# Kernel tuning notes

Hardware: AMD Instinct MI355X
Metric: run time of the kernel (lower is better)

The kernel has to match this reference:

```python
import jax, jax.numpy as jnp
import numpy as np

T, B, I, H = 512, 64, 256, 512

def setup_inputs() -> dict:
    key = jax.random.key(0)
    ks = jax.random.split(key, 5)
    s = 0.1  # matches uniform(-0.1, 0.1) init scale
    return {
        "x": jax.random.normal(ks[0], (T, B, I), dtype=jnp.float32),
        "weight_ih": jax.random.uniform(ks[1], (H, I), dtype=jnp.float32, minval=-s, maxval=s),
        "weight_hh": jax.random.uniform(ks[2], (H, H), dtype=jnp.float32, minval=-s, maxval=s),
        "bias_ih": jax.random.uniform(ks[3], (H,), dtype=jnp.float32, minval=-s, maxval=s),
        "bias_hh": jax.random.uniform(ks[4], (H,), dtype=jnp.float32, minval=-s, maxval=s),
    }

def reference(x, weight_ih, weight_hh, bias_ih, bias_hh):
    # Precompute input contribution for all timesteps in one big GEMM: [T,B,H]
    xw = jnp.einsum('tbi,hi->tbh', x, weight_ih) + bias_ih + bias_hh
    h0 = jnp.zeros((x.shape[1], weight_hh.shape[0]), dtype=x.dtype)

    def step(h, xw_t):
        h = jax.nn.relu(xw_t + h @ weight_hh.T)
        return h, h

    h_final, output = jax.lax.scan(step, h0, xw)
    return output, h_final
```

## Files before the change

### kernel.cpp

```cpp
#include <hip/hip_runtime.h>

#define T_DIM 512
#define B_DIM 64
#define I_DIM 256
#define H_DIM 512
#define BH_DIM (B_DIM * H_DIM)

__global__ __launch_bounds__(512, 2) void rnn_fused(
    const float* __restrict__ x, const float* __restrict__ wih,
    const float* __restrict__ whh, const float* __restrict__ bih,
    const float* __restrict__ bhh, float* __restrict__ out,
    unsigned long long* __restrict__ stage) {
  __shared__ __align__(16) float4 wihs4[128 * 64];
  __shared__ __align__(16) float hbuf[2][H_DIM];
  __shared__ __align__(16) float4 xbuf4[3 * 64];

  const int b   = blockIdx.x & 63;
  const int rb  = blockIdx.x >> 6;
  const int tid = threadIdx.x;
  const int rg  = tid >> 4;
  const int cg  = tid & 15;
  const int j0  = rb * 128 + rg * 4;

  const int pj = (tid < rb * 128) ? tid : tid + 128;

  float4 w[4][8];
#pragma unroll
  for (int r = 0; r < 4; r++) {
    const float4* wr = (const float4*)(whh + (size_t)(j0 + r) * H_DIM);
#pragma unroll
    for (int i = 0; i < 8; i++) w[r][i] = wr[i * 16 + cg];
  }

  {
    const float4* wg = (const float4*)(wih + (size_t)rb * 128 * I_DIM);
#pragma unroll
    for (int q = 0; q < 16; q++) {
      const int idx = q * 512 + tid;
      wihs4[idx] = wg[idx];
    }
  }

  const float4* xg = (const float4*)x;
  if (tid < 64) {
    xbuf4[0 * 64 + tid] = xg[((size_t)0 * B_DIM + b) * 64 + tid];
    xbuf4[1 * 64 + tid] = xg[((size_t)1 * B_DIM + b) * 64 + tid];
  }

  float bias = 0.f;
  if (cg < 4) bias = bih[j0 + cg] + bhh[j0 + cg];

  float* __restrict__ outb = out + (size_t)b * H_DIM;
  unsigned long long* __restrict__ stg0 = stage + (size_t)b * H_DIM;
  unsigned long long* __restrict__ stg1 = stage + (size_t)(64 + b) * H_DIM;

  __syncthreads();

  float hlast = 0.f;

  {
    float b0 = 0.f, b1 = 0.f, b2 = 0.f, b3 = 0.f;
    const float4* xb = &xbuf4[0];
    const float4* wr = &wihs4[(rg * 4) * 64];
#pragma unroll
    for (int i = 0; i < 4; i++) {
      const float4 xv = xb[i * 16 + cg];
      const float4 q0 = wr[0 * 64 + i * 16 + cg];
      const float4 q1 = wr[1 * 64 + i * 16 + cg];
      const float4 q2 = wr[2 * 64 + i * 16 + cg];
      const float4 q3 = wr[3 * 64 + i * 16 + cg];
      b0 = fmaf(q0.x, xv.x, b0); b0 = fmaf(q0.y, xv.y, b0);
      b0 = fmaf(q0.z, xv.z, b0); b0 = fmaf(q0.w, xv.w, b0);
      b1 = fmaf(q1.x, xv.x, b1); b1 = fmaf(q1.y, xv.y, b1);
      b1 = fmaf(q1.z, xv.z, b1); b1 = fmaf(q1.w, xv.w, b1);
      b2 = fmaf(q2.x, xv.x, b2); b2 = fmaf(q2.y, xv.y, b2);
      b2 = fmaf(q2.z, xv.z, b2); b2 = fmaf(q2.w, xv.w, b2);
      b3 = fmaf(q3.x, xv.x, b3); b3 = fmaf(q3.y, xv.y, b3);
      b3 = fmaf(q3.z, xv.z, b3); b3 = fmaf(q3.w, xv.w, b3);
    }
#pragma unroll
    for (int m = 1; m <= 8; m <<= 1) {
      b0 += __shfl_xor(b0, m, 64);
      b1 += __shfl_xor(b1, m, 64);
      b2 += __shfl_xor(b2, m, 64);
      b3 += __shfl_xor(b3, m, 64);
    }
    if (cg < 4) {
      const float acc = (cg == 0) ? b0 : (cg == 1) ? b1 : (cg == 2) ? b2 : b3;
      const float h = fmaxf(acc + bias, 0.f);
      const int j = j0 + cg;
      union { float f; unsigned int u; } cv; cv.f = h;
      __hip_atomic_store(&stg0[j], (unsigned long long)cv.u,
                         __ATOMIC_RELAXED, __HIP_MEMORY_SCOPE_AGENT);
      outb[j] = h;
      hbuf[0][j] = h;
      hlast = h;
    }
    if (tid < 64) {
      xbuf4[2 * 64 + tid] = xg[((size_t)2 * B_DIM + b) * 64 + tid];
    }
  }

  for (int t = 1; t < T_DIM; t++) {
    const int p = (t - 1) & 1;
    float* hb = hbuf[p];
    float* o_t = outb + (size_t)t * BH_DIM;

    float b0 = 0.f, b1 = 0.f, b2 = 0.f, b3 = 0.f;
    {
      const float4* xb = &xbuf4[(t % 3) * 64];
      const float4* wr = &wihs4[(rg * 4) * 64];
#pragma unroll
      for (int i = 0; i < 4; i++) {
        const float4 xv = xb[i * 16 + cg];
        const float4 q0 = wr[0 * 64 + i * 16 + cg];
        const float4 q1 = wr[1 * 64 + i * 16 + cg];
        const float4 q2 = wr[2 * 64 + i * 16 + cg];
        const float4 q3 = wr[3 * 64 + i * 16 + cg];
        b0 = fmaf(q0.x, xv.x, b0); b0 = fmaf(q0.y, xv.y, b0);
        b0 = fmaf(q0.z, xv.z, b0); b0 = fmaf(q0.w, xv.w, b0);
        b1 = fmaf(q1.x, xv.x, b1); b1 = fmaf(q1.y, xv.y, b1);
        b1 = fmaf(q1.z, xv.z, b1); b1 = fmaf(q1.w, xv.w, b1);
        b2 = fmaf(q2.x, xv.x, b2); b2 = fmaf(q2.y, xv.y, b2);
        b2 = fmaf(q2.z, xv.z, b2); b2 = fmaf(q2.w, xv.w, b2);
        b3 = fmaf(q3.x, xv.x, b3); b3 = fmaf(q3.y, xv.y, b3);
        b3 = fmaf(q3.z, xv.z, b3); b3 = fmaf(q3.w, xv.w, b3);
      }
    }

    float4 xpf = make_float4(0.f, 0.f, 0.f, 0.f);
    const bool do_pf = (tid < 64) && (t + 2 < T_DIM);
    if (do_pf) xpf = xg[((size_t)(t + 2) * B_DIM + b) * 64 + tid];

    if (tid < 384) {
      unsigned long long* slot = (p ? stg1 : stg0) + pj;
      const unsigned int want = (unsigned int)(t - 1);
      unsigned long long v;
      do {
        v = __hip_atomic_load(slot, __ATOMIC_RELAXED, __HIP_MEMORY_SCOPE_AGENT);
      } while ((unsigned int)(v >> 32) != want);
      union { unsigned int u; float f; } cv; cv.u = (unsigned int)v;
      hb[pj] = cv.f;
    }

    __syncthreads();

    if (do_pf) xbuf4[((t + 2) % 3) * 64 + tid] = xpf;

    float a0 = b0, a1 = b1, a2 = b2, a3 = b3;
#pragma unroll
    for (int i = 0; i < 8; i++) {
      const float4 hv = ((const float4*)hb)[i * 16 + cg];
      a0 = fmaf(w[0][i].x, hv.x, a0); a0 = fmaf(w[0][i].y, hv.y, a0);
      a0 = fmaf(w[0][i].z, hv.z, a0); a0 = fmaf(w[0][i].w, hv.w, a0);
      a1 = fmaf(w[1][i].x, hv.x, a1); a1 = fmaf(w[1][i].y, hv.y, a1);
      a1 = fmaf(w[1][i].z, hv.z, a1); a1 = fmaf(w[1][i].w, hv.w, a1);
      a2 = fmaf(w[2][i].x, hv.x, a2); a2 = fmaf(w[2][i].y, hv.y, a2);
      a2 = fmaf(w[2][i].z, hv.z, a2); a2 = fmaf(w[2][i].w, hv.w, a2);
      a3 = fmaf(w[3][i].x, hv.x, a3); a3 = fmaf(w[3][i].y, hv.y, a3);
      a3 = fmaf(w[3][i].z, hv.z, a3); a3 = fmaf(w[3][i].w, hv.w, a3);
    }
#pragma unroll
    for (int m = 1; m <= 8; m <<= 1) {
      a0 += __shfl_xor(a0, m, 64);
      a1 += __shfl_xor(a1, m, 64);
      a2 += __shfl_xor(a2, m, 64);
      a3 += __shfl_xor(a3, m, 64);
    }

    if (cg < 4) {
      const float acc = (cg == 0) ? a0 : (cg == 1) ? a1 : (cg == 2) ? a2 : a3;
      const float h = fmaxf(acc + bias, 0.f);
      const int j = j0 + cg;
      union { float f; unsigned int u; } cv; cv.f = h;
      const unsigned long long tag = (unsigned long long)(unsigned int)t << 32;
      unsigned long long* sb = (t & 1) ? stg1 : stg0;
      __hip_atomic_store(&sb[j], tag | cv.u,
                         __ATOMIC_RELAXED, __HIP_MEMORY_SCOPE_AGENT);
      o_t[j] = h;
      hbuf[t & 1][j] = h;
      hlast = h;
    }
  }

  if (cg < 4) {
    out[(size_t)T_DIM * BH_DIM + (size_t)b * H_DIM + j0 + cg] = hlast;
  }
}

extern "C" void kernel_launch(void* const* d_in, const int* in_sizes, int n_in,
                              void* d_out, int out_size, void* d_ws, size_t ws_size,
                              hipStream_t stream) {
  const float* x   = (const float*)d_in[0];
  const float* wih = (const float*)d_in[1];
  const float* whh = (const float*)d_in[2];
  const float* bih = (const float*)d_in[3];
  const float* bhh = (const float*)d_in[4];
  float* out = (float*)d_out;
  unsigned long long* stage = (unsigned long long*)d_ws;

  rnn_fused<<<256, 512, 0, stream>>>(x, wih, whh, bih, bhh, out, stage);
}
```

Measured before the change: 939.1 us.

## Split hidden rows into 8 slices and interleave two batch rows per block

Each block now owns 64 hidden rows (8 row-blocks) for two batch elements instead of 128 rows for one. The two batch recurrences alternate within the step: the wait and matvec for batch A run, then those for batch B. This halves the per-block recurrent matvec work on the critical path and lets one batch's cross-block wait overlap the other's compute. The cost is more blocks to synchronise per batch row, more polling threads, two barriers per step and a wider shuffle reduction.

```diff
diff --git a/kernel.cpp b/kernel.cpp
--- a/kernel.cpp
+++ b/kernel.cpp
@@ -6,185 +6,266 @@
 #define H_DIM 512
 #define BH_DIM (B_DIM * H_DIM)
 
-__global__ __launch_bounds__(512, 2) void rnn_fused(
+__global__ __launch_bounds__(512, 2) void rnn_fused2(
     const float* __restrict__ x, const float* __restrict__ wih,
     const float* __restrict__ whh, const float* __restrict__ bih,
     const float* __restrict__ bhh, float* __restrict__ out,
     unsigned long long* __restrict__ stage) {
-  __shared__ __align__(16) float4 wihs4[128 * 64];
-  __shared__ __align__(16) float hbuf[2][H_DIM];
-  __shared__ __align__(16) float4 xbuf4[3 * 64];
-
-  const int b   = blockIdx.x & 63;
-  const int rb  = blockIdx.x >> 6;
+  __shared__ __align__(16) float4 wihs4[64 * 64];
+  __shared__ __align__(16) float hbuf[2][2][H_DIM];
+  __shared__ __align__(16) float4 xbuf4[2][3][64];
+
+  const int bg  = blockIdx.x & 31;
+  const int rb  = blockIdx.x >> 5;
+  const int bA  = bg;
+  const int bB  = bg + 32;
   const int tid = threadIdx.x;
-  const int rg  = tid >> 4;
-  const int cg  = tid & 15;
-  const int j0  = rb * 128 + rg * 4;
-
-  const int pj = (tid < rb * 128) ? tid : tid + 128;
-
-  float4 w[4][8];
+  const int rg  = tid >> 5;
+  const int cg  = tid & 31;
+  const int j0  = rb * 64 + rg * 4;
+
+  const int pj = (tid < rb * 64) ? tid : tid + 64;
+
+  float4 w[4][4];
 #pragma unroll
   for (int r = 0; r < 4; r++) {
     const float4* wr = (const float4*)(whh + (size_t)(j0 + r) * H_DIM);
 #pragma unroll
-    for (int i = 0; i < 8; i++) w[r][i] = wr[i * 16 + cg];
+    for (int i = 0; i < 4; i++) w[r][i] = wr[i * 32 + cg];
   }
 
   {
-    const float4* wg = (const float4*)(wih + (size_t)rb * 128 * I_DIM);
-#pragma unroll
-    for (int q = 0; q < 16; q++) {
-      const int idx = q * 512 + tid;
-      wihs4[idx] = wg[idx];
-    }
+    const float4* wg = (const float4*)(wih + (size_t)rb * 64 * I_DIM);
+#pragma unroll
+    for (int q = 0; q < 8; q++) wihs4[q * 512 + tid] = wg[q * 512 + tid];
   }
 
   const float4* xg = (const float4*)x;
-  if (tid < 64) {
-    xbuf4[0 * 64 + tid] = xg[((size_t)0 * B_DIM + b) * 64 + tid];
-    xbuf4[1 * 64 + tid] = xg[((size_t)1 * B_DIM + b) * 64 + tid];
+  if (tid < 128) {
+    const int ab = tid >> 6;
+    const int c  = tid & 63;
+    const int bb = ab ? bB : bA;
+    xbuf4[ab][0][c] = xg[((size_t)0 * B_DIM + bb) * 64 + c];
+    xbuf4[ab][1][c] = xg[((size_t)1 * B_DIM + bb) * 64 + c];
   }
 
   float bias = 0.f;
   if (cg < 4) bias = bih[j0 + cg] + bhh[j0 + cg];
 
-  float* __restrict__ outb = out + (size_t)b * H_DIM;
-  unsigned long long* __restrict__ stg0 = stage + (size_t)b * H_DIM;
-  unsigned long long* __restrict__ stg1 = stage + (size_t)(64 + b) * H_DIM;
+  float* __restrict__ outA = out + (size_t)bA * H_DIM;
+  float* __restrict__ outB = out + (size_t)bB * H_DIM;
+  unsigned long long* __restrict__ stgA0 = stage + (size_t)bA * H_DIM;
+  unsigned long long* __restrict__ stgA1 = stage + (size_t)(64 + bA) * H_DIM;
+  unsigned long long* __restrict__ stgB0 = stage + (size_t)bB * H_DIM;
+  unsigned long long* __restrict__ stgB1 = stage + (size_t)(64 + bB) * H_DIM;
 
   __syncthreads();
 
-  float hlast = 0.f;
+  float hlastA = 0.f, hlastB = 0.f;
 
   {
-    float b0 = 0.f, b1 = 0.f, b2 = 0.f, b3 = 0.f;
-    const float4* xb = &xbuf4[0];
+    float aA0 = 0.f, aA1 = 0.f, aA2 = 0.f, aA3 = 0.f;
+    float aB0 = 0.f, aB1 = 0.f, aB2 = 0.f, aB3 = 0.f;
     const float4* wr = &wihs4[(rg * 4) * 64];
-#pragma unroll
-    for (int i = 0; i < 4; i++) {
-      const float4 xv = xb[i * 16 + cg];
-      const float4 q0 = wr[0 * 64 + i * 16 + cg];
-      const float4 q1 = wr[1 * 64 + i * 16 + cg];
-      const float4 q2 = wr[2 * 64 + i * 16 + cg];
-      const float4 q3 = wr[3 * 64 + i * 16 + cg];
-      b0 = fmaf(q0.x, xv.x, b0); b0 = fmaf(q0.y, xv.y, b0);
-      b0 = fmaf(q0.z, xv.z, b0); b0 = fmaf(q0.w, xv.w, b0);
-      b1 = fmaf(q1.x, xv.x, b1); b1 = fmaf(q1.y, xv.y, b1);
-      b1 = fmaf(q1.z, xv.z, b1); b1 = fmaf(q1.w, xv.w, b1);
-      b2 = fmaf(q2.x, xv.x, b2); b2 = fmaf(q2.y, xv.y, b2);
-      b2 = fmaf(q2.z, xv.z, b2); b2 = fmaf(q2.w, xv.w, b2);
-      b3 = fmaf(q3.x, xv.x, b3); b3 = fmaf(q3.y, xv.y, b3);
-      b3 = fmaf(q3.z, xv.z, b3); b3 = fmaf(q3.w, xv.w, b3);
-    }
-#pragma unroll
-    for (int m = 1; m <= 8; m <<= 1) {
-      b0 += __shfl_xor(b0, m, 64);
-      b1 += __shfl_xor(b1, m, 64);
-      b2 += __shfl_xor(b2, m, 64);
-      b3 += __shfl_xor(b3, m, 64);
+    const float4* xa = &xbuf4[0][0][0];
+    const float4* xb = &xbuf4[1][0][0];
+#pragma unroll
+    for (int i = 0; i < 2; i++) {
+      const int q = i * 32 + cg;
+      const float4 xva = xa[q];
+      const float4 xvb = xb[q];
+      const float4 q0 = wr[0 * 64 + q];
+      const float4 q1 = wr[1 * 64 + q];
+      const float4 q2 = wr[2 * 64 + q];
+      const float4 q3 = wr[3 * 64 + q];
+      aA0 = fmaf(q0.x, xva.x, aA0); aA0 = fmaf(q0.y, xva.y, aA0);
+      aA0 = fmaf(q0.z, xva.z, aA0); aA0 = fmaf(q0.w, xva.w, aA0);
+      aA1 = fmaf(q1.x, xva.x, aA1); aA1 = fmaf(q1.y, xva.y, aA1);
+      aA1 = fmaf(q1.z, xva.z, aA1); aA1 = fmaf(q1.w, xva.w, aA1);
+      aA2 = fmaf(q2.x, xva.x, aA2); aA2 = fmaf(q2.y, xva.y, aA2);
+      aA2 = fmaf(q2.z, xva.z, aA2); aA2 = fmaf(q2.w, xva.w, aA2);
+      aA3 = fmaf(q3.x, xva.x, aA3); aA3 = fmaf(q3.y, xva.y, aA3);
+      aA3 = fmaf(q3.z, xva.z, aA3); aA3 = fmaf(q3.w, xva.w, aA3);
+      aB0 = fmaf(q0.x, xvb.x, aB0); aB0 = fmaf(q0.y, xvb.y, aB0);
+      aB0 = fmaf(q0.z, xvb.z, aB0); aB0 = fmaf(q0.w, xvb.w, aB0);
+      aB1 = fmaf(q1.x, xvb.x, aB1); aB1 = fmaf(q1.y, xvb.y, aB1);
+      aB1 = fmaf(q1.z, xvb.z, aB1); aB1 = fmaf(q1.w, xvb.w, aB1);
+      aB2 = fmaf(q2.x, xvb.x, aB2); aB2 = fmaf(q2.y, xvb.y, aB2);
+      aB2 = fmaf(q2.z, xvb.z, aB2); aB2 = fmaf(q2.w, xvb.w, aB2);
+      aB3 = fmaf(q3.x, xvb.x, aB3); aB3 = fmaf(q3.y, xvb.y, aB3);
+      aB3 = fmaf(q3.z, xvb.z, aB3); aB3 = fmaf(q3.w, xvb.w, aB3);
+    }
+#pragma unroll
+    for (int m = 1; m <= 16; m <<= 1) {
+      aA0 += __shfl_xor(aA0, m, 64); aA1 += __shfl_xor(aA1, m, 64);
+      aA2 += __shfl_xor(aA2, m, 64); aA3 += __shfl_xor(aA3, m, 64);
+      aB0 += __shfl_xor(aB0, m, 64); aB1 += __shfl_xor(aB1, m, 64);
+      aB2 += __shfl_xor(aB2, m, 64); aB3 += __shfl_xor(aB3, m, 64);
     }
     if (cg < 4) {
-      const float acc = (cg == 0) ? b0 : (cg == 1) ? b1 : (cg == 2) ? b2 : b3;
-      const float h = fmaxf(acc + bias, 0.f);
       const int j = j0 + cg;
-      union { float f; unsigned int u; } cv; cv.f = h;
-      __hip_atomic_store(&stg0[j], (unsigned long long)cv.u,
-                         __ATOMIC_RELAXED, __HIP_MEMORY_SCOPE_AGENT);
-      outb[j] = h;
-      hbuf[0][j] = h;
-      hlast = h;
-    }
-    if (tid < 64) {
-      xbuf4[2 * 64 + tid] = xg[((size_t)2 * B_DIM + b) * 64 + tid];
+      union { float f; unsigned int u; } cv;
+      const float accA = (cg == 0) ? aA0 : (cg == 1) ? aA1 : (cg == 2) ? aA2 : aA3;
+      const float hA = fmaxf(accA + bias, 0.f);
+      cv.f = hA;
+      __hip_atomic_store(&stgA0[j], (unsigned long long)cv.u,
+                         __ATOMIC_RELAXED, __HIP_MEMORY_SCOPE_AGENT);
+      outA[j] = hA; hbuf[0][0][j] = hA; hlastA = hA;
+      const float accB = (cg == 0) ? aB0 : (cg == 1) ? aB1 : (cg == 2) ? aB2 : aB3;
+      const float hB = fmaxf(accB + bias, 0.f);
+      cv.f = hB;
+      __hip_atomic_store(&stgB0[j], (unsigned long long)cv.u,
+                         __ATOMIC_RELAXED, __HIP_MEMORY_SCOPE_AGENT);
+      outB[j] = hB; hbuf[1][0][j] = hB; hlastB = hB;
+    }
+    if (tid < 128) {
+      const int ab = tid >> 6;
+      const int c  = tid & 63;
+      const int bb = ab ? bB : bA;
+      xbuf4[ab][2][c] = xg[((size_t)2 * B_DIM + bb) * 64 + c];
     }
   }
 
   for (int t = 1; t < T_DIM; t++) {
     const int p = (t - 1) & 1;
-    float* hb = hbuf[p];
-    float* o_t = outb + (size_t)t * BH_DIM;
-
-    float b0 = 0.f, b1 = 0.f, b2 = 0.f, b3 = 0.f;
+    const int s = t % 3;
+    float* o_tA = outA + (size_t)t * BH_DIM;
+    float* o_tB = outB + (size_t)t * BH_DIM;
+
+    float aA0 = 0.f, aA1 = 0.f, aA2 = 0.f, aA3 = 0.f;
+    float aB0 = 0.f, aB1 = 0.f, aB2 = 0.f, aB3 = 0.f;
     {
-      const float4* xb = &xbuf4[(t % 3) * 64];
       const float4* wr = &wihs4[(rg * 4) * 64];
-#pragma unroll
-      for (int i = 0; i < 4; i++) {
-        const float4 xv = xb[i * 16 + cg];
-        const float4 q0 = wr[0 * 64 + i * 16 + cg];
-        const float4 q1 = wr[1 * 64 + i * 16 + cg];
-        const float4 q2 = wr[2 * 64 + i * 16 + cg];
-        const float4 q3 = wr[3 * 64 + i * 16 + cg];
-        b0 = fmaf(q0.x, xv.x, b0); b0 = fmaf(q0.y, xv.y, b0);
-        b0 = fmaf(q0.z, xv.z, b0); b0 = fmaf(q0.w, xv.w, b0);
-        b1 = fmaf(q1.x, xv.x, b1); b1 = fmaf(q1.y, xv.y, b1);
-        b1 = fmaf(q1.z, xv.z, b1); b1 = fmaf(q1.w, xv.w, b1);
-        b2 = fmaf(q2.x, xv.x, b2); b2 = fmaf(q2.y, xv.y, b2);
-        b2 = fmaf(q2.z, xv.z, b2); b2 = fmaf(q2.w, xv.w, b2);
-        b3 = fmaf(q3.x, xv.x, b3); b3 = fmaf(q3.y, xv.y, b3);
-        b3 = fmaf(q3.z, xv.z, b3); b3 = fmaf(q3.w, xv.w, b3);
+      const float4* xa = &xbuf4[0][s][0];
+      const float4* xb = &xbuf4[1][s][0];
+#pragma unroll
+      for (int i = 0; i < 2; i++) {
+        const int q = i * 32 + cg;
+        const float4 xva = xa[q];
+        const float4 xvb = xb[q];
+        const float4 q0 = wr[0 * 64 + q];
+        const float4 q1 = wr[1 * 64 + q];
+        const float4 q2 = wr[2 * 64 + q];
+        const float4 q3 = wr[3 * 64 + q];
+        aA0 = fmaf(q0.x, xva.x, aA0); aA0 = fmaf(q0.y, xva.y, aA0);
+        aA0 = fmaf(q0.z, xva.z, aA0); aA0 = fmaf(q0.w, xva.w, aA0);
+        aA1 = fmaf(q1.x, xva.x, aA1); aA1 = fmaf(q1.y, xva.y, aA1);
+        aA1 = fmaf(q1.z, xva.z, aA1); aA1 = fmaf(q1.w, xva.w, aA1);
+        aA2 = fmaf(q2.x, xva.x, aA2); aA2 = fmaf(q2.y, xva.y, aA2);
+        aA2 = fmaf(q2.z, xva.z, aA2); aA2 = fmaf(q2.w, xva.w, aA2);
+        aA3 = fmaf(q3.x, xva.x, aA3); aA3 = fmaf(q3.y, xva.y, aA3);
+        aA3 = fmaf(q3.z, xva.z, aA3); aA3 = fmaf(q3.w, xva.w, aA3);
+        aB0 = fmaf(q0.x, xvb.x, aB0); aB0 = fmaf(q0.y, xvb.y, aB0);
+        aB0 = fmaf(q0.z, xvb.z, aB0); aB0 = fmaf(q0.w, xvb.w, aB0);
+        aB1 = fmaf(q1.x, xvb.x, aB1); aB1 = fmaf(q1.y, xvb.y, aB1);
+        aB1 = fmaf(q1.z, xvb.z, aB1); aB1 = fmaf(q1.w, xvb.w, aB1);
+        aB2 = fmaf(q2.x, xvb.x, aB2); aB2 = fmaf(q2.y, xvb.y, aB2);
+        aB2 = fmaf(q2.z, xvb.z, aB2); aB2 = fmaf(q2.w, xvb.w, aB2);
+        aB3 = fmaf(q3.x, xvb.x, aB3); aB3 = fmaf(q3.y, xvb.y, aB3);
+        aB3 = fmaf(q3.z, xvb.z, aB3); aB3 = fmaf(q3.w, xvb.w, aB3);
       }
     }
 
     float4 xpf = make_float4(0.f, 0.f, 0.f, 0.f);
-    const bool do_pf = (tid < 64) && (t + 2 < T_DIM);
-    if (do_pf) xpf = xg[((size_t)(t + 2) * B_DIM + b) * 64 + tid];
-
-    if (tid < 384) {
-      unsigned long long* slot = (p ? stg1 : stg0) + pj;
+    const bool do_pf = (tid < 128) && (t + 2 < T_DIM);
+    if (do_pf) {
+      const int bb = (tid < 64) ? bA : bB;
+      xpf = xg[((size_t)(t + 2) * B_DIM + bb) * 64 + (tid & 63)];
+    }
+
+    if (tid < 448) {
+      unsigned long long* slot = (p ? stgA1 : stgA0) + pj;
       const unsigned int want = (unsigned int)(t - 1);
       unsigned long long v;
       do {
         v = __hip_atomic_load(slot, __ATOMIC_RELAXED, __HIP_MEMORY_SCOPE_AGENT);
       } while ((unsigned int)(v >> 32) != want);
       union { unsigned int u; float f; } cv; cv.u = (unsigned int)v;
-      hb[pj] = cv.f;
-    }
-
+      hbuf[0][p][pj] = cv.f;
+    }
     __syncthreads();
 
-    if (do_pf) xbuf4[((t + 2) % 3) * 64 + tid] = xpf;
-
-    float a0 = b0, a1 = b1, a2 = b2, a3 = b3;
-#pragma unroll
-    for (int i = 0; i < 8; i++) {
-      const float4 hv = ((const float4*)hb)[i * 16 + cg];
-      a0 = fmaf(w[0][i].x, hv.x, a0); a0 = fmaf(w[0][i].y, hv.y, a0);
-      a0 = fmaf(w[0][i].z, hv.z, a0); a0 = fmaf(w[0][i].w, hv.w, a0);
-      a1 = fmaf(w[1][i].x, hv.x, a1); a1 = fmaf(w[1][i].y, hv.y, a1);
-      a1 = fmaf(w[1][i].z, hv.z, a1); a1 = fmaf(w[1][i].w, hv.w, a1);
-      a2 = fmaf(w[2][i].x, hv.x, a2); a2 = fmaf(w[2][i].y, hv.y, a2);
-      a2 = fmaf(w[2][i].z, hv.z, a2); a2 = fmaf(w[2][i].w, hv.w, a2);
-      a3 = fmaf(w[3][i].x, hv.x, a3); a3 = fmaf(w[3][i].y, hv.y, a3);
-      a3 = fmaf(w[3][i].z, hv.z, a3); a3 = fmaf(w[3][i].w, hv.w, a3);
-    }
-#pragma unroll
-    for (int m = 1; m <= 8; m <<= 1) {
-      a0 += __shfl_xor(a0, m, 64);
-      a1 += __shfl_xor(a1, m, 64);
-      a2 += __shfl_xor(a2, m, 64);
-      a3 += __shfl_xor(a3, m, 64);
-    }
-
+    if (do_pf) xbuf4[tid >> 6][(t + 2) % 3][tid & 63] = xpf;
+
+    {
+      const float* hbp = hbuf[0][p];
+#pragma unroll
+      for (int i = 0; i < 4; i++) {
+        const float4 hv = ((const float4*)hbp)[i * 32 + cg];
+        aA0 = fmaf(w[0][i].x, hv.x, aA0); aA0 = fmaf(w[0][i].y, hv.y, aA0);
+        aA0 = fmaf(w[0][i].z, hv.z, aA0); aA0 = fmaf(w[0][i].w, hv.w, aA0);
+        aA1 = fmaf(w[1][i].x, hv.x, aA1); aA1 = fmaf(w[1][i].y, hv.y, aA1);
+        aA1 = fmaf(w[1][i].z, hv.z, aA1); aA1 = fmaf(w[1][i].w, hv.w, aA1);
+        aA2 = fmaf(w[2][i].x, hv.x, aA2); aA2 = fmaf(w[2][i].y, hv.y, aA2);
+        aA2 = fmaf(w[2][i].z, hv.z, aA2); aA2 = fmaf(w[2][i].w, hv.w, aA2);
+        aA3 = fmaf(w[3][i].x, hv.x, aA3); aA3 = fmaf(w[3][i].y, hv.y, aA3);
+        aA3 = fmaf(w[3][i].z, hv.z, aA3); aA3 = fmaf(w[3][i].w, hv.w, aA3);
+      }
+    }
+#pragma unroll
+    for (int m = 1; m <= 16; m <<= 1) {
+      aA0 += __shfl_xor(aA0, m, 64); aA1 += __shfl_xor(aA1, m, 64);
+      aA2 += __shfl_xor(aA2, m, 64); aA3 += __shfl_xor(aA3, m, 64);
+    }
     if (cg < 4) {
-      const float acc = (cg == 0) ? a0 : (cg == 1) ? a1 : (cg == 2) ? a2 : a3;
+      const float acc = (cg == 0) ? aA0 : (cg == 1) ? aA1 : (cg == 2) ? aA2 : aA3;
       const float h = fmaxf(acc + bias, 0.f);
       const int j = j0 + cg;
       union { float f; unsigned int u; } cv; cv.f = h;
       const unsigned long long tag = (unsigned long long)(unsigned int)t << 32;
-      unsigned long long* sb = (t & 1) ? stg1 : stg0;
-      __hip_atomic_store(&sb[j], tag | cv.u,
-                         __ATOMIC_RELAXED, __HIP_MEMORY_SCOPE_AGENT);
-      o_t[j] = h;
-      hbuf[t & 1][j] = h;
-      hlast = h;
+      __hip_atomic_store(&((t & 1) ? stgA1 : stgA0)[j], tag | cv.u,
+                         __ATOMIC_RELAXED, __HIP_MEMORY_SCOPE_AGENT);
+      o_tA[j] = h; hbuf[0][t & 1][j] = h; hlastA = h;
+    }
+
+    if (tid < 448) {
+      unsigned long long* slot = (p ? stgB1 : stgB0) + pj;
+      const unsigned int want = (unsigned int)(t - 1);
+      unsigned long long v;
+      do {
+        v = __hip_atomic_load(slot, __ATOMIC_RELAXED, __HIP_MEMORY_SCOPE_AGENT);
+      } while ((unsigned int)(v >> 32) != want);
+      union { unsigned int u; float f; } cv; cv.u = (unsigned int)v;
+      hbuf[1][p][pj] = cv.f;
+    }
+    __syncthreads();
+
+    {
+      const float* hbp = hbuf[1][p];
+#pragma unroll
+      for (int i = 0; i < 4; i++) {
+        const float4 hv = ((const float4*)hbp)[i * 32 + cg];
+        aB0 = fmaf(w[0][i].x, hv.x, aB0); aB0 = fmaf(w[0][i].y, hv.y, aB0);
+        aB0 = fmaf(w[0][i].z, hv.z, aB0); aB0 = fmaf(w[0][i].w, hv.w, aB0);
+        aB1 = fmaf(w[1][i].x, hv.x, aB1); aB1 = fmaf(w[1][i].y, hv.y, aB1);
+        aB1 = fmaf(w[1][i].z, hv.z, aB1); aB1 = fmaf(w[1][i].w, hv.w, aB1);
+        aB2 = fmaf(w[2][i].x, hv.x, aB2); aB2 = fmaf(w[2][i].y, hv.y, aB2);
+        aB2 = fmaf(w[2][i].z, hv.z, aB2); aB2 = fmaf(w[2][i].w, hv.w, aB2);
+        aB3 = fmaf(w[3][i].x, hv.x, aB3); aB3 = fmaf(w[3][i].y, hv.y, aB3);
+        aB3 = fmaf(w[3][i].z, hv.z, aB3); aB3 = fmaf(w[3][i].w, hv.w, aB3);
+      }
+    }
+#pragma unroll
+    for (int m = 1; m <= 16; m <<= 1) {
+      aB0 += __shfl_xor(aB0, m, 64); aB1 += __shfl_xor(aB1, m, 64);
+      aB2 += __shfl_xor(aB2, m, 64); aB3 += __shfl_xor(aB3, m, 64);
+    }
+    if (cg < 4) {
+      const float acc = (cg == 0) ? aB0 : (cg == 1) ? aB1 : (cg == 2) ? aB2 : aB3;
+      const float h = fmaxf(acc + bias, 0.f);
+      const int j = j0 + cg;
+      union { float f; unsigned int u; } cv; cv.f = h;
+      const unsigned long long tag = (unsigned long long)(unsigned int)t << 32;
+      __hip_atomic_store(&((t & 1) ? stgB1 : stgB0)[j], tag | cv.u,
+                         __ATOMIC_RELAXED, __HIP_MEMORY_SCOPE_AGENT);
+      o_tB[j] = h; hbuf[1][t & 1][j] = h; hlastB = h;
     }
   }
 
   if (cg < 4) {
-    out[(size_t)T_DIM * BH_DIM + (size_t)b * H_DIM + j0 + cg] = hlast;
+    const int j = j0 + cg;
+    out[(size_t)T_DIM * BH_DIM + (size_t)bA * H_DIM + j] = hlastA;
+    out[(size_t)T_DIM * BH_DIM + (size_t)bB * H_DIM + j] = hlastB;
   }
 }
 
@@ -199,5 +280,5 @@
   float* out = (float*)d_out;
   unsigned long long* stage = (unsigned long long*)d_ws;
 
-  rnn_fused<<<256, 512, 0, stream>>>(x, wih, whh, bih, bhh, out, stage);
+  rnn_fused2<<<256, 512, 0, stream>>>(x, wih, whh, bih, bhh, out, stage);
 }
```

Result: slower. 1.280 ms (+36.3%).
